# Kernel optimization log

Hardware: AMD Instinct MI355X
Metric: run time of the kernel (lower is better)

## Reference

```python
import jax, jax.numpy as jnp
import numpy as np

B, S, W, T = 16, 32, 32, 64
H2 = 512   # num_hidden*2: decoder state / encoder state size
Hf = 256   # vocab_nn hidden (= num_hidden)
F = 128    # vectorizer.vector_size
A = 128    # attn_hidden (= num_hidden // 2)
V = 32000  # vocab size; distribution over V+1 (last slot = OOV / -1 index)


def setup_inputs() -> dict:
    key = jax.random.key(0)
    ks = jax.random.split(key, 24)
    p = lambda k, shp, s=0.05: (jax.random.normal(k, shp) * s).astype(jnp.float32)
    d = {}
    d["text_states"] = p(ks[0], (B, S, W, H2), 0.5)
    d["sentence_states"] = p(ks[1], (B, S, H2), 0.5)
    d["text_length"] = jnp.clip(jax.random.randint(ks[2], (B, S), 0, W), 1, W)
    d["state"] = p(ks[3], (B, 2, H2), 0.5)
    d["summary"] = jax.random.randint(ks[4], (B, T), 0, V)
    d["summary_length"] = jnp.clip(jax.random.randint(ks[5], (B,), 0, T), 2, T)
    d["emb"] = p(ks[6], (V + 1, F), 0.02)            # vectorizer embedding
    d["W_cc"] = p(ks[7], (F + H2, F)); d["b_cc"] = jnp.zeros((F,), jnp.float32)
    d["Wx"] = p(ks[8], (F, 4 * H2)); d["Wh"] = p(ks[9], (H2, 4 * H2))
    d["b_lstm"] = jnp.zeros((4 * H2,), jnp.float32)
    d["W_a"] = p(ks[10], (2 * H2 + 1, A)); d["b_a"] = jnp.zeros((A,), jnp.float32)
    d["v_a"] = p(ks[11], (A,))
    d["W_rc"] = p(ks[12], (2 * H2, H2)); d["b_rc"] = jnp.zeros((H2,), jnp.float32)
    d["W1"] = p(ks[13], (2 * H2, Hf)); d["b1"] = jnp.zeros((Hf,), jnp.float32)
    d["W2"] = p(ks[14], (Hf, V + 1)); d["b2"] = jnp.zeros((V + 1,), jnp.float32)
    return d


def reference(text_states, sentence_states, text_length, state, summary,
              summary_length, emb, W_cc, b_cc, Wx, Wh, b_lstm,
              W_a, b_a, v_a, W_rc, b_rc, W1, b1, W2, b2):
    SW = S * W
    ws = text_states.reshape(B, SW, H2)  # word states, flattened source positions
    ss = jnp.broadcast_to(sentence_states[:, :, None, :], (B, S, W, H2)).reshape(B, SW, H2)
    cat_states = jnp.concatenate([ws, ss], -1)               # (B,SW,4H)
    mask = (jnp.arange(W) < text_length[:, :, None]).reshape(B, SW)
    Wa_word, Wa_out, wa_cov = W_a[:H2], W_a[H2:2 * H2], W_a[2 * H2]
    ws_a = ws @ Wa_word + b_a                                # step-invariant, (B,SW,A)

    def step(carry, xs):
        st, coverage, ctx, loss = carry
        tok_t, tok_tp1, t = xs
        valid = ((summary_length - t - 1) > 0).astype(jnp.float32)
        # CombineContext + LSTM decoder cell
        x = jnp.concatenate([emb[tok_t], ctx], 1) @ W_cc + b_cc
        h, c = st[:, 0], st[:, 1]
        gi, gf, gg, go = jnp.split(x @ Wx + h @ Wh + b_lstm, 4, axis=1)
        c_new = jax.nn.sigmoid(gf) * c + jax.nn.sigmoid(gi) * jnp.tanh(gg)
        out = jax.nn.sigmoid(go) * jnp.tanh(c_new)           # (B,2H)
        # hierarchical attention with coverage feature (input dim 4H+1)
        scores = jnp.tanh(ws_a + (out @ Wa_out)[:, None, :]
                          + coverage[:, :, None] * wa_cov) @ v_a
        attn = jax.nn.softmax(jnp.where(mask, scores, -1e9), axis=1)
        ctx4 = jnp.einsum('bn,bnd->bd', attn, cat_states)    # (B,4H)
        ctx_new = ctx4 @ W_rc + b_rc                         # ReduceContextVector -> (B,2H)
        # vocabulary distribution
        hid = jax.nn.relu(jnp.concatenate([ctx_new, out], 1) @ W1 + b1)
        vocab = jax.nn.softmax(hid @ W2 + b2, axis=1)        # (B,V+1)
        tgt = jnp.where(tok_tp1 == -1, V, tok_tp1)           # map_input_indices_
        logp = jnp.log(jnp.take_along_axis(vocab, tgt[:, None], 1)[:, 0])
        covloss = jnp.minimum(coverage, attn).sum(1)
        loss = loss + valid * (-logp + covloss)              # gamma = 1
        # scatter-back semantics of timestep_wrapper: invalid rows zeroed
        attn_m = attn * valid[:, None]
        st_new = jnp.stack([out, c_new], 1) * valid[:, None, None]
        return (st_new, coverage + attn_m, ctx_new * valid[:, None], loss), None

    coverage0 = jnp.zeros((B, SW), jnp.float32)
    ctx0 = jnp.zeros((B, H2), jnp.float32)
    loss0 = jnp.zeros((B,), jnp.float32)
    xs = (summary[:, :-1].T, summary[:, 1:].T, jnp.arange(T - 1))
    (_, _, _, loss), _ = jax.lax.scan(step, (state, coverage0, ctx0, loss0), xs)
    return loss / (summary_length.astype(jnp.float32) - 1.0)
```

## Files before the change

kernel.cpp:

```cpp
#include <hip/hip_runtime.h>
#include <math.h>

#define B 16
#define S 32
#define T 64
#define H2 512
#define Hf 256
#define F 128
#define A 128
#define V 32000
#define SW 1024
#define NSTEP 63
#define VP1 32001
#define NBLK 256

__device__ __forceinline__ float frcp(float x){ return __builtin_amdgcn_rcpf(x); }
__device__ __forceinline__ float fsigm(float x){ return frcp(1.f + __expf(-x)); }
__device__ __forceinline__ float ftanh_(float x){
    float e = __expf(-2.f*fabsf(x));
    float t = (1.f - e)*frcp(1.f + e);
    return x >= 0.f ? t : -t;
}
__device__ __forceinline__ void ast(float* p, float v){
    __hip_atomic_store(p, v, __ATOMIC_RELAXED, __HIP_MEMORY_SCOPE_AGENT);
}
__device__ __forceinline__ unsigned bfr(float x){
    unsigned u = __float_as_uint(x);
    return (u + 0x7fffu + ((u >> 16) & 1u)) >> 16;
}
__device__ __forceinline__ float blo(unsigned u){ return __uint_as_float(u << 16); }
__device__ __forceinline__ float bhi(unsigned u){ return __uint_as_float(u & 0xffff0000u); }

__device__ __forceinline__ void gbar(unsigned* arr, unsigned* rel, unsigned gen){
    asm volatile("s_waitcnt vmcnt(0) lgkmcnt(0)" ::: "memory");
    __syncthreads();
    if (blockIdx.x == 0){
        if (threadIdx.x > 0 && threadIdx.x < NBLK){
            while (__hip_atomic_load(&arr[threadIdx.x*32], __ATOMIC_RELAXED,
                                     __HIP_MEMORY_SCOPE_AGENT) < gen)
                __builtin_amdgcn_s_sleep(2);
        }
        __syncthreads();
        if (threadIdx.x == 0)
            __hip_atomic_store(rel, gen, __ATOMIC_RELAXED, __HIP_MEMORY_SCOPE_AGENT);
        __syncthreads();
    } else {
        if (threadIdx.x == 0){
            __hip_atomic_store(&arr[blockIdx.x*32], gen, __ATOMIC_RELAXED,
                               __HIP_MEMORY_SCOPE_AGENT);
            while (__hip_atomic_load(rel, __ATOMIC_RELAXED,
                                     __HIP_MEMORY_SCOPE_AGENT) < gen)
                __builtin_amdgcn_s_sleep(4);
        }
        __syncthreads();
    }
}

__global__ __launch_bounds__(256) void k_init0(
    const float* __restrict__ emb, const float* __restrict__ W_cc,
    const float* __restrict__ b_cc, const int* __restrict__ summary,
    float* __restrict__ xR, unsigned* __restrict__ cnt)
{
    int blk = blockIdx.x, tid = threadIdx.x;
    if (blk < 16){
        int b = blk;
        int tok = summary[b*T + 0];
        if (tid < F){
            float a = 0.f;
            for (int k = 0; k < F; ++k) a += emb[(size_t)tok*F + k]*W_cc[(size_t)k*F + tid];
            xR[b*F + tid] = a + b_cc[tid];
        }
    } else {
        for (int i = tid; i < 8256; i += 256) cnt[i] = 0u;
    }
}

__global__ __launch_bounds__(256) void k_wsa(
    const float* __restrict__ ws, const float* __restrict__ W_a, const float* __restrict__ b_a,
    float* __restrict__ ws_aT)
{
    __shared__ float wss2[512][20];
    int b = blockIdx.x, nt = blockIdx.y, tid = threadIdx.x;
    int n0 = nt*16;
    const float* wsrc = ws + ((size_t)(b*SW + n0))*H2;
    for (int i = tid; i < 16*512; i += 256){
        int n_l = i >> 9, k = i & 511;
        wss2[k][n_l] = wsrc[i];
    }
    __syncthreads();
    int a = tid & 127, nh = tid >> 7;
    float acc[8];
    float ba = b_a[a];
    #pragma unroll
    for (int j = 0; j < 8; ++j) acc[j] = ba;
    for (int k = 0; k < H2; ++k){
        float wa = W_a[k*A + a];
        const float4 u0 = *(const float4*)&wss2[k][nh*8];
        const float4 u1 = *(const float4*)&wss2[k][nh*8 + 4];
        acc[0] += u0.x*wa; acc[1] += u0.y*wa; acc[2] += u0.z*wa; acc[3] += u0.w*wa;
        acc[4] += u1.x*wa; acc[5] += u1.y*wa; acc[6] += u1.z*wa; acc[7] += u1.w*wa;
    }
    float* dst = ws_aT + ((size_t)(b*A + a))*SW + n0 + nh*8;
    #pragma unroll
    for (int j = 0; j < 8; ++j) dst[j] = acc[j];
}

__global__ __launch_bounds__(256) void k_wf(
    const float* __restrict__ W_rc, const float* __restrict__ b_rc,
    const float* __restrict__ W1, const float* __restrict__ b1,
    const float* __restrict__ W_cc,
    float* __restrict__ Wf, float* __restrict__ bf, float* __restrict__ bconst)
{
    __shared__ float wrc[4][512];
    int j = blockIdx.x, tid = threadIdx.x;
    if (j < 256){
        for (int i = tid; i < 2048; i += 256){
            int kk = i >> 9, r = i & 511;
            wrc[kk][r] = W_rc[((size_t)(j*4 + kk))*H2 + r];
        }
        __syncthreads();
        float a0=0,a1=0,a2=0,a3=0;
        for (int r = 0; r < 512; ++r){
            float w1 = W1[(size_t)r*Hf + tid];
            a0 += wrc[0][r]*w1; a1 += wrc[1][r]*w1; a2 += wrc[2][r]*w1; a3 += wrc[3][r]*w1;
        }
        Wf[((size_t)(j*4+0))*Hf + tid] = a0;
        Wf[((size_t)(j*4+1))*Hf + tid] = a1;
        Wf[((size_t)(j*4+2))*Hf + tid] = a2;
        Wf[((size_t)(j*4+3))*Hf + tid] = a3;
    } else {
        float acc = b1[tid];
        for (int r = 0; r < 512; ++r) acc += b_rc[r]*W1[(size_t)r*Hf + tid];
        bf[tid] = acc;
        if (tid < 128){
            float a = 0.f;
            for (int c = 0; c < H2; ++c) a += b_rc[c]*W_cc[(size_t)(F+c)*F + tid];
            bconst[tid] = a;
        }
    }
}

__global__ __launch_bounds__(128) void k_wrcc(
    const float* __restrict__ W_rc, const float* __restrict__ W_cc, float* __restrict__ WRCC)
{
    __shared__ float wr[512];
    int d = blockIdx.x, f = threadIdx.x;
    for (int i = f; i < 512; i += 128) wr[i] = W_rc[(size_t)d*H2 + i];
    __syncthreads();
    float a = 0.f;
    for (int c = 0; c < H2; ++c) a += wr[c]*W_cc[(size_t)(F+c)*F + f];
    WRCC[(size_t)d*F + f] = a;
}

__global__ __launch_bounds__(128) void k_embx(
    const int* __restrict__ summary, const float* __restrict__ emb,
    const float* __restrict__ W_cc, const float* __restrict__ b_cc,
    float* __restrict__ embx)
{
    __shared__ float er[128];
    int t = blockIdx.x, b = blockIdx.y, f = threadIdx.x;
    int tok = summary[b*T + t];
    er[f] = emb[(size_t)tok*F + f];
    __syncthreads();
    float a = b_cc[f];
    for (int k = 0; k < F; ++k) a += er[k]*W_cc[(size_t)k*F + f];
    embx[((size_t)t*B + b)*F + f] = a;
}

__global__ __launch_bounds__(1024) void k_packw2(
    const float* __restrict__ W2, unsigned* __restrict__ W2h)
{
    size_t idx = (size_t)blockIdx.x*1024 + threadIdx.x;
    int rp = (int)(idx >> 15), v = (int)(idx & 32767);
    float lo = (v < VP1) ? W2[(size_t)(2*rp)*VP1 + v] : 0.f;
    float hi = (v < VP1) ? W2[(size_t)(2*rp+1)*VP1 + v] : 0.f;
    W2h[idx] = bfr(lo) | (bfr(hi) << 16);
}
__global__ __launch_bounds__(1024) void k_packws(
    const float* __restrict__ ws, unsigned* __restrict__ wsh)
{
    size_t idx = (size_t)blockIdx.x*1024 + threadIdx.x;
    int b = (int)(idx >> 18), r = (int)(idx & 262143);
    int np = r >> 9, d = r & 511;
    float lo = ws[((size_t)b*SW + 2*np)*H2 + d];
    float hi = ws[((size_t)b*SW + 2*np+1)*H2 + d];
    wsh[idx] = bfr(lo) | (bfr(hi) << 16);
}
__global__ __launch_bounds__(1024) void k_packwsa(
    const float* __restrict__ ws_aT, unsigned* __restrict__ ws_aTh)
{
    size_t idx = (size_t)blockIdx.x*1024 + threadIdx.x;
    int b = (int)(idx >> 16), r = (int)(idx & 65535);
    int ap = r >> 10, n = r & 1023;
    float lo = ws_aT[((size_t)b*A + 2*ap)*SW + n];
    float hi = ws_aT[((size_t)b*A + 2*ap+1)*SW + n];
    ws_aTh[idx] = bfr(lo) | (bfr(hi) << 16);
}
__global__ __launch_bounds__(1024) void k_packwg(
    const float* __restrict__ Wx, const float* __restrict__ Wh,
    unsigned* __restrict__ wgh)
{
    size_t idx = (size_t)blockIdx.x*1024 + threadIdx.x;
    int kp = (int)(idx >> 11), cg = (int)(idx & 2047);
    int k0 = 2*kp, k1 = 2*kp + 1;
    float lo = (k0 < F) ? Wx[(size_t)k0*2048 + cg] : Wh[(size_t)(k0-F)*2048 + cg];
    float hi = (k1 < F) ? Wx[(size_t)k1*2048 + cg] : Wh[(size_t)(k1-F)*2048 + cg];
    wgh[idx] = bfr(lo) | (bfr(hi) << 16);
}

__global__ __launch_bounds__(512, 2) void k_persist(
    const float* __restrict__ ss,
    const int* __restrict__ text_length, const int* __restrict__ summary,
    const int* __restrict__ sumlen, const float* __restrict__ state,
    const unsigned* __restrict__ wgh, const float* __restrict__ b_lstm,
    const float* __restrict__ W_a, const float* __restrict__ v_a,
    const float* __restrict__ W1, const float* __restrict__ b2,
    const unsigned* __restrict__ W2h, const unsigned* __restrict__ wsh,
    const unsigned* __restrict__ ws_aTh,
    const float* __restrict__ Wf, const float* __restrict__ bf,
    const float* __restrict__ WRCC, const float* __restrict__ bconst,
    const float* __restrict__ embx,
    float* xR, float* outR, float* hidR, float* scoresR, float* c4R,
    float* woR, float* mpartR, float* spartR, float* m2R, float* s2R,
    float* tgtlogR, float* covlpR, float* d_out, unsigned* cnt)
{
    __shared__ unsigned W2L[16384];
    __shared__ unsigned wsaL[4096];
    __shared__ float BIG[15104];
    __shared__ float woOL[512];
    __shared__ float redS[576];
    __shared__ float red2[528];
    __shared__ float wo_l[128];
    __shared__ float wac_l[128], vas_l[128], b2_l[128];
    __shared__ float score_l[64], cov_l[64];
    __shared__ float c_l[128];
    __shared__ float gsum[528];
    __shared__ float asum_l[32];
    __shared__ float mred[136], sred[136], msc2[16];
    __shared__ float loss_l[16];
    __shared__ float misc[4];
    __shared__ int tl_l[32], sumlen_l[16], tgt_l[16];

    const int blk = blockIdx.x, tid = threadIdx.x;
    const int b_role = blk >> 4, sl = blk & 15;
    unsigned* arr = cnt;
    unsigned* rel = cnt + 8192;

    const int vl = tid & 127, rq = tid >> 7;
    const int dl = tid & 31, nq = tid >> 5;
    const int n3 = tid & 63, aq = tid >> 6;
    const int cc = tid & 31, kg = tid >> 5;

    unsigned wsr[32];
    #pragma unroll
    for (int j = 0; j < 32; ++j)
        wsr[j] = wsh[((size_t)b_role*512 + nq*32 + j)*512 + sl*32 + dl];
    unsigned wgr[20];
    if (blk < 64){
        const int CGg = (cc >> 3)*512 + blk*8 + (cc & 7);
        #pragma unroll
        for (int j = 0; j < 20; ++j)
            wgr[j] = wgh[(size_t)(kg*20 + j)*2048 + CGg];
    }
    #pragma unroll
    for (int q = 0; q < 32; ++q){
        int i = q*512 + tid;
        W2L[i] = W2h[(size_t)(i >> 7)*32768 + blk*128 + (i & 127)];
    }
    #pragma unroll
    for (int q = 0; q < 8; ++q){
        int i = q*512 + tid;
        wsaL[i] = ws_aTh[((size_t)(b_role*64 + (i >> 6)))*1024 + sl*64 + (i & 63)];
    }

    if (tid < 128){
        wac_l[tid] = W_a[(size_t)(2*H2)*A + tid];
        vas_l[tid] = v_a[tid];
        int v2 = blk*128 + tid;
        b2_l[tid] = (v2 < VP1) ? b2[v2] : 0.f;
    }
    if (tid < 32) tl_l[tid] = text_length[b_role*S + tid];
    if (tid < 16){ sumlen_l[tid] = sumlen[tid]; loss_l[tid] = 0.f; }
    if (tid < 64) cov_l[tid] = 0.f;
    if (blk < 64 && tid < 128){
        int b = tid >> 3, c = tid & 7;
        c_l[tid] = state[(size_t)b*2*H2 + H2 + blk*8 + c];
    }
    __syncthreads();

    unsigned gen = 0;
    for (int t = 0; t <= NSTEP; ++t){
        if (t >= 1){
            if (tid < 16) mred[tid] = mpartR[(size_t)(t-1)*256 + b_role*16 + tid];
            if (tid >= 16 && tid < 32) mred[tid] = spartR[(size_t)(t-1)*256 + b_role*16 + (tid-16)];
            __syncthreads();
            if (tid == 0){
                float M = -1e30f;
                for (int i = 0; i < 16; ++i) M = fmaxf(M, mred[i]);
                float Sv = 0.f;
                for (int i = 0; i < 16; ++i) Sv += mred[16+i]*__expf(mred[i]-M);
                misc[0] = M; misc[1] = frcp(Sv);
            }
            __syncthreads();
            if (tid < 64){
                float at = __expf(score_l[tid]-misc[0])*misc[1];
                float clp = fminf(cov_l[tid], at);
                float vm1 = (sumlen_l[b_role] - t > 0) ? 1.f : 0.f;
                cov_l[tid] += at*vm1;
                sred[tid] = clp;
            }
            __syncthreads();
            if (tid == 0){
                float s = 0.f;
                for (int i = 0; i < 64; ++i) s += sred[i];
                ast(&covlpR[(size_t)(t-1)*256 + b_role*16 + sl], s);
            }
            __syncthreads();
        }
        if (t < NSTEP && blk < 64){
            float* xh = BIG;
            const float* xb0 = xR + (size_t)t*B*F;
            const float* hb0 = outR + (size_t)(t > 0 ? t-1 : 0)*B*H2;
            #pragma unroll
            for (int q = 0; q < 20; ++q){
                int i = q*512 + tid;
                int b = i/640, k = i - b*640;
                float v;
                if (k < F) v = xb0[b*F + k];
                else if (t == 0) v = state[(size_t)b*2*H2 + (k - F)];
                else v = hb0[b*H2 + (k - F)] * ((sumlen_l[b] - t > 0) ? 1.f : 0.f);
                xh[i] = v;
            }
            __syncthreads();
            for (int b = 0; b < 16; ++b){
                const float* xb = &BIG[b*640 + kg*40];
                float s0 = 0.f, s1 = 0.f;
                #pragma unroll
                for (int j = 0; j < 20; ++j){
                    unsigned wu = wgr[j];
                    s0 = fmaf(xb[2*j],   blo(wu), s0);
                    s1 = fmaf(xb[2*j+1], bhi(wu), s1);
                }
                float p = s0 + s1;
                p += __shfl_xor(p, 32);
                if ((kg & 1) == 0)
                    BIG[10240 + (b*8 + (kg >> 1))*32 + cc] = p;
            }
            __syncthreads();
            {
                int b = tid >> 5, c2 = tid & 31;
                float s = 0.f;
                #pragma unroll
                for (int q = 0; q < 8; ++q) s += BIG[10240 + (b*8 + q)*32 + c2];
                gsum[b*33 + c2] = s;
            }
            __syncthreads();
            if (tid < 128){
                int b = tid >> 3, c = tid & 7, col = blk*8 + c;
                float gi = gsum[b*33 + c]      + b_lstm[col];
                float gf = gsum[b*33 + 8 + c]  + b_lstm[H2 + col];
                float gg = gsum[b*33 + 16 + c] + b_lstm[2*H2 + col];
                float go = gsum[b*33 + 24 + c] + b_lstm[3*H2 + col];
                float cold = c_l[tid];
                float cn = fsigm(gf)*cold + fsigm(gi)*ftanh_(gg);
                float o = fsigm(go)*ftanh_(cn);
                float valid = (sumlen_l[b] - t - 1 > 0) ? 1.f : 0.f;
                c_l[tid] = cn*valid;
                ast(&outR[(size_t)t*B*H2 + b*H2 + col], o);
            }
        }
        gen++; gbar(arr, rel, gen);

        if (t >= 1){
            if (tid < 16){ int tok = summary[tid*T + t]; tgt_l[tid] = (tok == -1) ? V : tok; }
            #pragma unroll
            for (int q = 0; q < 8; ++q){
                int idx = q*512 + tid;
                int r = idx >> 4, b = idx & 15;
                BIG[b*264 + r] = hidR[(size_t)(t-1)*B*Hf + idx];
            }
            __syncthreads();
            unsigned wreg[32];
            #pragma unroll
            for (int i = 0; i < 32; ++i) wreg[i] = W2L[(rq*32 + i)*128 + vl];
            for (int b = 0; b < 16; ++b){
                const float2* hb2 = (const float2*)&BIG[b*264 + rq*64];
                float a0 = 0.f, a1 = 0.f;
                #pragma unroll
                for (int i = 0; i < 32; ++i){
                    unsigned u = wreg[i];
                    float2 h = hb2[i];
                    a0 = fmaf(h.x, blo(u), a0);
                    a1 = fmaf(h.y, bhi(u), a1);
                }
                BIG[4224 + rq*2176 + vl*17 + b] = a0 + a1;
            }
            __syncthreads();
            #pragma unroll
            for (int j = 0; j < 4; ++j){
                int idx = tid*4 + j;
                int vl2 = idx >> 4, bb = idx & 15;
                float s = BIG[4224 + 0*2176 + vl2*17 + bb]
                        + BIG[4224 + 1*2176 + vl2*17 + bb]
                        + BIG[4224 + 2*2176 + vl2*17 + bb]
                        + BIG[4224 + 3*2176 + vl2*17 + bb];
                int v2 = blk*128 + vl2;
                float lg = (v2 < VP1) ? (s + b2_l[vl2]) : -1e30f;
                if (v2 < VP1 && v2 == tgt_l[bb])
                    ast(&tgtlogR[(size_t)(t-1)*16 + bb], lg);
                BIG[12928 + vl2*17 + bb] = lg;
            }
            __syncthreads();
            if (tid < 128){
                int b2i = tid & 15, grp = tid >> 4;
                float m = -1e30f;
                #pragma unroll
                for (int i = 0; i < 16; ++i) m = fmaxf(m, BIG[12928 + (grp*16+i)*17 + b2i]);
                mred[grp*17 + b2i] = m;
            }
            __syncthreads();
            if (tid < 16){
                float m = -1e30f;
                #pragma unroll
                for (int q = 0; q < 8; ++q) m = fmaxf(m, mred[q*17 + tid]);
                msc2[tid] = m;
            }
            __syncthreads();
            if (tid < 128){
                int b2i = tid & 15, grp = tid >> 4;
                float Mb = msc2[b2i];
                float s = 0.f;
                #pragma unroll
                for (int i = 0; i < 16; ++i) s += __expf(BIG[12928 + (grp*16+i)*17 + b2i] - Mb);
                sred[grp*17 + b2i] = s;
            }
            __syncthreads();
            if (tid < 16){
                float s = 0.f;
                #pragma unroll
                for (int q = 0; q < 8; ++q) s += sred[q*17 + tid];
                ast(&m2R[(size_t)(t-1)*B*256 + tid*256 + blk], msc2[tid]);
                ast(&s2R[(size_t)(t-1)*B*256 + tid*256 + blk], s);
            }
        }
        if (t < NSTEP && blk >= 128){
            int idx = blk - 128, bwo = idx >> 3, ah = idx & 7;
            woOL[tid] = outR[(size_t)t*B*H2 + bwo*H2 + tid];
            __syncthreads();
            {
                int a16 = tid & 15, kq2 = tid >> 4;
                float acc = 0.f;
                #pragma unroll
                for (int j = 0; j < 16; ++j){
                    int k = kq2*16 + j;
                    acc = fmaf(woOL[k], W_a[(size_t)(H2 + k)*A + ah*16 + a16], acc);
                }
                red2[a16*33 + kq2] = acc;
            }
            __syncthreads();
            if (tid < 16){
                float s = 0.f;
                #pragma unroll
                for (int q = 0; q < 32; ++q) s += red2[tid*33 + q];
                ast(&woR[(size_t)t*B*A + bwo*128 + ah*16 + tid], s);
            }
        }
        gen++; gbar(arr, rel, gen);

        if (t == NSTEP){
            if (blk == 255 && tid < 256){
                int tf = NSTEP - 1;
                int bb = tid >> 4, g = tid & 15;
                float mv[16];
                float m = -1e30f;
                #pragma unroll
                for (int j = 0; j < 16; ++j){
                    mv[j] = m2R[(size_t)tf*B*256 + bb*256 + g + j*16];
                    m = fmaxf(m, mv[j]);
                }
                #pragma unroll
                for (int off = 1; off < 16; off <<= 1) m = fmaxf(m, __shfl_xor(m, off, 16));
                float s = 0.f;
                #pragma unroll
                for (int j = 0; j < 16; ++j)
                    s += s2R[(size_t)tf*B*256 + bb*256 + g + j*16]*__expf(mv[j]-m);
                #pragma unroll
                for (int off = 1; off < 16; off <<= 1) s += __shfl_xor(s, off, 16);
                if (g == 0){
                    float cl = 0.f;
                    for (int q = 0; q < 16; ++q) cl += covlpR[(size_t)tf*256 + bb*16 + q];
                    float tlg = tgtlogR[(size_t)tf*16 + bb];
                    float logp = tlg - m - __logf(s);
                    float vld = (sumlen_l[bb] - tf - 1 > 0) ? 1.f : 0.f;
                    loss_l[bb] += vld*(-logp + cl);
                    d_out[bb] = loss_l[bb] / ((float)sumlen_l[bb] - 1.f);
                }
            }
            break;
        }

        {
            if (tid < 128) wo_l[tid] = woR[(size_t)t*B*A + b_role*128 + tid];
            __syncthreads();
            {
                float cv = cov_l[n3];
                float acc = 0.f;
                #pragma unroll
                for (int i = 0; i < 8; ++i){
                    unsigned u = wsaL[(aq*8 + i)*64 + n3];
                    int a0 = aq*16 + 2*i;
                    acc = fmaf(ftanh_(blo(u) + wo_l[a0] + cv*wac_l[a0]), vas_l[a0], acc);
                    acc = fmaf(ftanh_(bhi(u) + wo_l[a0+1] + cv*wac_l[a0+1]), vas_l[a0+1], acc);
                }
                redS[aq*72 + n3] = acc;
            }
            __syncthreads();
            if (tid < 64){
                float s = 0.f;
                #pragma unroll
                for (int q = 0; q < 8; ++q) s += redS[q*72 + tid];
                int nn = sl*64 + tid;
                float sc = ((nn & 31) < tl_l[nn >> 5]) ? s : -1e9f;
                score_l[tid] = sc;
                ast(&scoresR[(size_t)t*B*SW + b_role*SW + nn], sc);
            }
            __syncthreads();
            if (tid == 0){
                float m = score_l[0];
                for (int i = 1; i < 64; ++i) m = fmaxf(m, score_l[i]);
                float s = 0.f;
                for (int i = 0; i < 64; ++i) s += __expf(score_l[i]-m);
                ast(&mpartR[(size_t)t*256 + b_role*16 + sl], m);
                ast(&spartR[(size_t)t*256 + b_role*16 + sl], s);
            }
        }
        gen++; gbar(arr, rel, gen);

        {
            float* SC = BIG;
            float* AT = BIG + 1024;
            float* redc = BIG + 2048;
            #pragma unroll
            for (int q = 0; q < 2; ++q)
                SC[q*512 + tid] = scoresR[(size_t)t*B*SW + b_role*SW + q*512 + tid];
            if (tid < 16) mred[tid] = mpartR[(size_t)t*256 + b_role*16 + tid];
            if (tid >= 16 && tid < 32) mred[tid] = spartR[(size_t)t*256 + b_role*16 + (tid-16)];
            __syncthreads();
            if (tid == 0){
                float M = -1e30f;
                for (int i = 0; i < 16; ++i) M = fmaxf(M, mred[i]);
                float Sv = 0.f;
                for (int i = 0; i < 16; ++i) Sv += mred[16+i]*__expf(mred[i]-M);
                misc[0] = M; misc[1] = frcp(Sv);
            }
            __syncthreads();
            #pragma unroll
            for (int q = 0; q < 2; ++q){
                int n = q*512 + tid;
                AT[n] = __expf(SC[n]-misc[0])*misc[1];
            }
            __syncthreads();
            if (tid < 32){
                float s = 0.f;
                #pragma unroll
                for (int j = 0; j < 32; ++j) s += AT[tid*32 + ((j + tid) & 31)];
                asum_l[tid] = s;
            }
            {
                float acc0 = 0.f, acc1 = 0.f;
                const float2* at2 = (const float2*)&AT[nq*64];
                #pragma unroll
                for (int j = 0; j < 32; ++j){
                    unsigned u = wsr[j];
                    float2 av = at2[j];
                    acc0 = fmaf(av.x, blo(u), acc0);
                    acc1 = fmaf(av.y, bhi(u), acc1);
                }
                redc[nq*32 + dl] = acc0 + acc1;
            }
            __syncthreads();
            if (tid < 32){
                float s = 0.f;
                #pragma unroll
                for (int q = 0; q < 16; ++q) s += redc[q*32 + tid];
                ast(&c4R[(size_t)t*B*SW + b_role*SW + sl*32 + tid], s);
            } else if (tid < 64){
                int d2 = tid - 32;
                float s = 0.f;
                const float* ssb = ss + ((size_t)(b_role*S))*H2 + sl*32 + d2;
                #pragma unroll 4
                for (int s2 = 0; s2 < 32; ++s2)
                    s = fmaf(asum_l[s2], ssb[(size_t)s2*H2], s);
                ast(&c4R[(size_t)t*B*SW + b_role*SW + 512 + sl*32 + d2], s);
            }
        }
        gen++; gbar(arr, rel, gen);

        if (sl < 12){
            float* c4l = BIG;
            float* OL  = BIG + 1024;
            float* redd = BIG + 1536;
            #pragma unroll
            for (int q = 0; q < 2; ++q)
                c4l[q*512 + tid] = c4R[(size_t)t*B*SW + b_role*SW + q*512 + tid];
            if (tid < 512) OL[tid] = outR[(size_t)t*B*H2 + b_role*H2 + tid];
            __syncthreads();
            int cl = tid & 31, kq = tid >> 5;
            if (sl < 8){
                int col = sl*32 + cl;
                float acc = 0.f;
                const float* wp = Wf + (size_t)(kq*64)*Hf + col;
                #pragma unroll 4
                for (int i = 0; i < 64; ++i)
                    acc = fmaf(c4l[kq*64+i], wp[(size_t)i*Hf], acc);
                const float* w1p = W1 + (size_t)(H2 + kq*32)*Hf + col;
                #pragma unroll 4
                for (int i = 0; i < 32; ++i)
                    acc = fmaf(OL[kq*32+i], w1p[(size_t)i*Hf], acc);
                redd[kq*32 + cl] = acc;
                __syncthreads();
                if (tid < 32){
                    float z = 0.f;
                    #pragma unroll
                    for (int q = 0; q < 16; ++q) z += redd[q*32 + tid];
                    z += bf[sl*32 + tid];
                    ast(&hidR[(size_t)t*B*Hf + (sl*32 + tid)*16 + b_role], fmaxf(z, 0.f));
                }
            } else {
                int f = (sl-8)*32 + cl;
                float acc = 0.f;
                const float* wp = WRCC + (size_t)(kq*64)*F + f;
                #pragma unroll 4
                for (int i = 0; i < 64; ++i)
                    acc = fmaf(c4l[kq*64+i], wp[(size_t)i*F], acc);
                redd[kq*32 + cl] = acc;
                __syncthreads();
                if (tid < 32){
                    int f2 = (sl-8)*32 + tid;
                    float z = 0.f;
                    #pragma unroll
                    for (int q = 0; q < 16; ++q) z += redd[q*32 + tid];
                    float vld = (sumlen_l[b_role] - t - 1 > 0) ? 1.f : 0.f;
                    float xv = embx[((size_t)(t+1)*B + b_role)*F + f2] + vld*(z + bconst[f2]);
                    ast(&xR[(size_t)(t+1)*B*F + b_role*F + f2], xv);
                }
            }
        }
        if (t >= 1 && blk == 255 && tid < 256){
            int tf = t - 1;
            int bb = tid >> 4, g = tid & 15;
            float mv[16];
            float m = -1e30f;
            #pragma unroll
            for (int j = 0; j < 16; ++j){
                mv[j] = m2R[(size_t)tf*B*256 + bb*256 + g + j*16];
                m = fmaxf(m, mv[j]);
            }
            #pragma unroll
            for (int off = 1; off < 16; off <<= 1) m = fmaxf(m, __shfl_xor(m, off, 16));
            float s = 0.f;
            #pragma unroll
            for (int j = 0; j < 16; ++j)
                s += s2R[(size_t)tf*B*256 + bb*256 + g + j*16]*__expf(mv[j]-m);
            #pragma unroll
            for (int off = 1; off < 16; off <<= 1) s += __shfl_xor(s, off, 16);
            if (g == 0){
                float cl = 0.f;
                for (int q = 0; q < 16; ++q) cl += covlpR[(size_t)tf*256 + bb*16 + q];
                float tlg = tgtlogR[(size_t)tf*16 + bb];
                float logp = tlg - m - __logf(s);
                float vld = (sumlen_l[bb] - tf - 1 > 0) ? 1.f : 0.f;
                loss_l[bb] += vld*(-logp + cl);
            }
        }
        gen++; gbar(arr, rel, gen);
    }
}

extern "C" void kernel_launch(void* const* d_in, const int* in_sizes, int n_in,
                              void* d_out, int out_size, void* d_ws, size_t ws_size,
                              hipStream_t stream) {
    const float* text_states = (const float*)d_in[0];
    const float* sent_states = (const float*)d_in[1];
    const int*   text_length = (const int*)d_in[2];
    const float* state       = (const float*)d_in[3];
    const int*   summary     = (const int*)d_in[4];
    const int*   sumlen      = (const int*)d_in[5];
    const float* emb    = (const float*)d_in[6];
    const float* W_cc   = (const float*)d_in[7];
    const float* b_cc   = (const float*)d_in[8];
    const float* Wx     = (const float*)d_in[9];
    const float* Wh     = (const float*)d_in[10];
    const float* b_lstm = (const float*)d_in[11];
    const float* W_a    = (const float*)d_in[12];
    const float* b_a    = (const float*)d_in[13];
    const float* v_a    = (const float*)d_in[14];
    const float* W_rc   = (const float*)d_in[15];
    const float* b_rc   = (const float*)d_in[16];
    const float* W1     = (const float*)d_in[17];
    const float* b1     = (const float*)d_in[18];
    const float* W2     = (const float*)d_in[19];
    const float* b2     = (const float*)d_in[20];
    float* out = (float*)d_out;

    float* p = (float*)d_ws;
    float* ws_aT   = p; p += (size_t)B*A*SW;
    float* Wf      = p; p += (size_t)1024*Hf;
    float* bfv     = p; p += Hf;
    float* WRCC    = p; p += (size_t)1024*F;
    float* bconst  = p; p += F;
    float* embx    = p; p += (size_t)T*B*F;
    float* xR      = p; p += (size_t)(NSTEP+1)*B*F;
    float* outR    = p; p += (size_t)(NSTEP+1)*B*H2;
    float* hidR    = p; p += (size_t)(NSTEP+1)*B*Hf;
    float* scoresR = p; p += (size_t)(NSTEP+1)*B*SW;
    float* c4R     = p; p += (size_t)(NSTEP+1)*B*SW;
    float* woR     = p; p += (size_t)(NSTEP+1)*B*A;
    float* mpartR  = p; p += (size_t)(NSTEP+1)*256;
    float* spartR  = p; p += (size_t)(NSTEP+1)*256;
    float* m2R     = p; p += (size_t)(NSTEP+1)*B*256;
    float* s2R     = p; p += (size_t)(NSTEP+1)*B*256;
    float* tgtlogR = p; p += (size_t)(NSTEP+1)*16;
    float* covlpR  = p; p += (size_t)(NSTEP+1)*256;
    unsigned* cnt  = (unsigned*)p; p += 8256;
    unsigned* W2h    = (unsigned*)p; p += (size_t)128*32768;
    unsigned* wsh    = (unsigned*)p; p += (size_t)16*512*512;
    unsigned* ws_aTh = (unsigned*)p; p += (size_t)16*64*1024;
    unsigned* wgh    = (unsigned*)p; p += (size_t)320*2048;

    k_init0<<<17, 256, 0, stream>>>(emb, W_cc, b_cc, summary, xR, cnt);
    k_wsa<<<dim3(B, 64), 256, 0, stream>>>(text_states, W_a, b_a, ws_aT);
    k_wf<<<257, 256, 0, stream>>>(W_rc, b_rc, W1, b1, W_cc, Wf, bfv, bconst);
    k_wrcc<<<1024, 128, 0, stream>>>(W_rc, W_cc, WRCC);
    k_embx<<<dim3(T, B), 128, 0, stream>>>(summary, emb, W_cc, b_cc, embx);
    k_packw2<<<4096, 1024, 0, stream>>>(W2, W2h);
    k_packws<<<4096, 1024, 0, stream>>>(text_states, wsh);
    k_packwsa<<<1024, 1024, 0, stream>>>(ws_aT, ws_aTh);
    k_packwg<<<640, 1024, 0, stream>>>(Wx, Wh, wgh);
    k_persist<<<NBLK, 512, 0, stream>>>(
        sent_states, text_length, summary, sumlen, state,
        wgh, b_lstm, W_a, v_a, W1, b2,
        W2h, wsh, ws_aTh, Wf, bfv, WRCC, bconst, embx,
        xR, outR, hidR, scoresR, c4R, woR, mpartR, spartR, m2R, s2R,
        tgtlogR, covlpR, out, cnt);
}
```

Before: 4.692 ms.

## Fuse out@W_a into LSTM stage and merge vocab phase to drop grid barriers

The LSTM blocks now compute their partial out·W_a products right after producing their slice of the hidden state and write bf16-packed partials. The attention blocks reduce those partials directly, so the separate wo phase and its grid barrier go away. The vocab-logit/softmax-partial work moves into the same phase as the attention context, which removes one more barrier per step. The barrier release flag is spread over 8 cache lines and the spin sleeps are shortened. In exchange, wo is rounded through bf16 and the scratch buffer grows.

Result: faster. 4.489 ms (-4.3%).

```diff
diff --git a/kernel.cpp b/kernel.cpp
--- a/kernel.cpp
+++ b/kernel.cpp
@@ -24,6 +24,9 @@
 __device__ __forceinline__ void ast(float* p, float v){
     __hip_atomic_store(p, v, __ATOMIC_RELAXED, __HIP_MEMORY_SCOPE_AGENT);
 }
+__device__ __forceinline__ void astu(unsigned* p, unsigned v){
+    __hip_atomic_store(p, v, __ATOMIC_RELAXED, __HIP_MEMORY_SCOPE_AGENT);
+}
 __device__ __forceinline__ unsigned bfr(float x){
     unsigned u = __float_as_uint(x);
     return (u + 0x7fffu + ((u >> 16) & 1u)) >> 16;
@@ -38,19 +41,20 @@
         if (threadIdx.x > 0 && threadIdx.x < NBLK){
             while (__hip_atomic_load(&arr[threadIdx.x*32], __ATOMIC_RELAXED,
                                      __HIP_MEMORY_SCOPE_AGENT) < gen)
-                __builtin_amdgcn_s_sleep(2);
+                __builtin_amdgcn_s_sleep(1);
         }
         __syncthreads();
-        if (threadIdx.x == 0)
-            __hip_atomic_store(rel, gen, __ATOMIC_RELAXED, __HIP_MEMORY_SCOPE_AGENT);
+        if (threadIdx.x < 8)
+            __hip_atomic_store(&rel[threadIdx.x*32], gen, __ATOMIC_RELAXED,
+                               __HIP_MEMORY_SCOPE_AGENT);
         __syncthreads();
     } else {
         if (threadIdx.x == 0){
             __hip_atomic_store(&arr[blockIdx.x*32], gen, __ATOMIC_RELAXED,
                                __HIP_MEMORY_SCOPE_AGENT);
-            while (__hip_atomic_load(rel, __ATOMIC_RELAXED,
+            while (__hip_atomic_load(&rel[(blockIdx.x & 7)*32], __ATOMIC_RELAXED,
                                      __HIP_MEMORY_SCOPE_AGENT) < gen)
-                __builtin_amdgcn_s_sleep(4);
+                __builtin_amdgcn_s_sleep(1);
         }
         __syncthreads();
     }
@@ -71,7 +75,7 @@
             xR[b*F + tid] = a + b_cc[tid];
         }
     } else {
-        for (int i = tid; i < 8256; i += 256) cnt[i] = 0u;
+        for (int i = tid; i < 8704; i += 256) cnt[i] = 0u;
     }
 }
 
@@ -221,13 +225,12 @@
     const float* __restrict__ WRCC, const float* __restrict__ bconst,
     const float* __restrict__ embx,
     float* xR, float* outR, float* hidR, float* scoresR, float* c4R,
-    float* woR, float* mpartR, float* spartR, float* m2R, float* s2R,
+    unsigned* wopartH, float* mpartR, float* spartR, float* m2R, float* s2R,
     float* tgtlogR, float* covlpR, float* d_out, unsigned* cnt)
 {
     __shared__ unsigned W2L[16384];
     __shared__ unsigned wsaL[4096];
-    __shared__ float BIG[15104];
-    __shared__ float woOL[512];
+    __shared__ float BIG[15552];
     __shared__ float redS[576];
     __shared__ float red2[528];
     __shared__ float wo_l[128];
@@ -319,6 +322,13 @@
         }
         if (t < NSTEP && blk < 64){
             float* xh = BIG;
+            float* outloc = BIG + 14336;
+            float* waL = BIG + 14464;
+            {
+                int i2 = tid*2;
+                waL[i2]   = W_a[(size_t)(H2 + blk*8 + (i2 >> 7))*A + (i2 & 127)];
+                waL[i2+1] = W_a[(size_t)(H2 + blk*8 + ((i2+1) >> 7))*A + ((i2+1) & 127)];
+            }
             const float* xb0 = xR + (size_t)t*B*F;
             const float* hb0 = outR + (size_t)(t > 0 ? t-1 : 0)*B*H2;
             #pragma unroll
@@ -366,141 +376,51 @@
                 float o = fsigm(go)*ftanh_(cn);
                 float valid = (sumlen_l[b] - t - 1 > 0) ? 1.f : 0.f;
                 c_l[tid] = cn*valid;
+                outloc[tid] = o;
                 ast(&outR[(size_t)t*B*H2 + b*H2 + col], o);
             }
+            __syncthreads();
+            {
+                int o2 = tid*2;
+                int b = o2 >> 6, ap0 = o2 & 63;
+                #pragma unroll
+                for (int w = 0; w < 2; ++w){
+                    int ap = ap0 + w, a0 = ap*2;
+                    float acc0 = 0.f, acc1 = 0.f;
+                    #pragma unroll
+                    for (int j = 0; j < 8; ++j){
+                        float ov = outloc[b*8 + j];
+                        acc0 = fmaf(ov, waL[j*128 + a0],     acc0);
+                        acc1 = fmaf(ov, waL[j*128 + a0 + 1], acc1);
+                    }
+                    astu(&wopartH[(size_t)t*65536 + blk*1024 + b*64 + ap],
+                         bfr(acc0) | (bfr(acc1) << 16));
+                }
+            }
         }
         gen++; gbar(arr, rel, gen);
 
-        if (t >= 1){
-            if (tid < 16){ int tok = summary[tid*T + t]; tgt_l[tid] = (tok == -1) ? V : tok; }
-            #pragma unroll
-            for (int q = 0; q < 8; ++q){
-                int idx = q*512 + tid;
-                int r = idx >> 4, b = idx & 15;
-                BIG[b*264 + r] = hidR[(size_t)(t-1)*B*Hf + idx];
-            }
-            __syncthreads();
-            unsigned wreg[32];
-            #pragma unroll
-            for (int i = 0; i < 32; ++i) wreg[i] = W2L[(rq*32 + i)*128 + vl];
-            for (int b = 0; b < 16; ++b){
-                const float2* hb2 = (const float2*)&BIG[b*264 + rq*64];
-                float a0 = 0.f, a1 = 0.f;
-                #pragma unroll
-                for (int i = 0; i < 32; ++i){
-                    unsigned u = wreg[i];
-                    float2 h = hb2[i];
-                    a0 = fmaf(h.x, blo(u), a0);
-                    a1 = fmaf(h.y, bhi(u), a1);
-                }
-                BIG[4224 + rq*2176 + vl*17 + b] = a0 + a1;
-            }
-            __syncthreads();
-            #pragma unroll
-            for (int j = 0; j < 4; ++j){
-                int idx = tid*4 + j;
-                int vl2 = idx >> 4, bb = idx & 15;
-                float s = BIG[4224 + 0*2176 + vl2*17 + bb]
-                        + BIG[4224 + 1*2176 + vl2*17 + bb]
-                        + BIG[4224 + 2*2176 + vl2*17 + bb]
-                        + BIG[4224 + 3*2176 + vl2*17 + bb];
-                int v2 = blk*128 + vl2;
-                float lg = (v2 < VP1) ? (s + b2_l[vl2]) : -1e30f;
-                if (v2 < VP1 && v2 == tgt_l[bb])
-                    ast(&tgtlogR[(size_t)(t-1)*16 + bb], lg);
-                BIG[12928 + vl2*17 + bb] = lg;
-            }
-            __syncthreads();
-            if (tid < 128){
-                int b2i = tid & 15, grp = tid >> 4;
-                float m = -1e30f;
-                #pragma unroll
-                for (int i = 0; i < 16; ++i) m = fmaxf(m, BIG[12928 + (grp*16+i)*17 + b2i]);
-                mred[grp*17 + b2i] = m;
-            }
-            __syncthreads();
-            if (tid < 16){
-                float m = -1e30f;
-                #pragma unroll
-                for (int q = 0; q < 8; ++q) m = fmaxf(m, mred[q*17 + tid]);
-                msc2[tid] = m;
-            }
-            __syncthreads();
-            if (tid < 128){
-                int b2i = tid & 15, grp = tid >> 4;
-                float Mb = msc2[b2i];
-                float s = 0.f;
-                #pragma unroll
-                for (int i = 0; i < 16; ++i) s += __expf(BIG[12928 + (grp*16+i)*17 + b2i] - Mb);
-                sred[grp*17 + b2i] = s;
-            }
-            __syncthreads();
-            if (tid < 16){
-                float s = 0.f;
-                #pragma unroll
-                for (int q = 0; q < 8; ++q) s += sred[q*17 + tid];
-                ast(&m2R[(size_t)(t-1)*B*256 + tid*256 + blk], msc2[tid]);
-                ast(&s2R[(size_t)(t-1)*B*256 + tid*256 + blk], s);
-            }
-        }
-        if (t < NSTEP && blk >= 128){
-            int idx = blk - 128, bwo = idx >> 3, ah = idx & 7;
-            woOL[tid] = outR[(size_t)t*B*H2 + bwo*H2 + tid];
-            __syncthreads();
+        if (t < NSTEP){
             {
-                int a16 = tid & 15, kq2 = tid >> 4;
-                float acc = 0.f;
-                #pragma unroll
-                for (int j = 0; j < 16; ++j){
-                    int k = kq2*16 + j;
-                    acc = fmaf(woOL[k], W_a[(size_t)(H2 + k)*A + ah*16 + a16], acc);
-                }
-                red2[a16*33 + kq2] = acc;
-            }
-            __syncthreads();
-            if (tid < 16){
-                float s = 0.f;
-                #pragma unroll
-                for (int q = 0; q < 32; ++q) s += red2[tid*33 + q];
-                ast(&woR[(size_t)t*B*A + bwo*128 + ah*16 + tid], s);
-            }
-        }
-        gen++; gbar(arr, rel, gen);
-
-        if (t == NSTEP){
-            if (blk == 255 && tid < 256){
-                int tf = NSTEP - 1;
-                int bb = tid >> 4, g = tid & 15;
-                float mv[16];
-                float m = -1e30f;
-                #pragma unroll
-                for (int j = 0; j < 16; ++j){
-                    mv[j] = m2R[(size_t)tf*B*256 + bb*256 + g + j*16];
-                    m = fmaxf(m, mv[j]);
-                }
-                #pragma unroll
-                for (int off = 1; off < 16; off <<= 1) m = fmaxf(m, __shfl_xor(m, off, 16));
-                float s = 0.f;
-                #pragma unroll
-                for (int j = 0; j < 16; ++j)
-                    s += s2R[(size_t)tf*B*256 + bb*256 + g + j*16]*__expf(mv[j]-m);
-                #pragma unroll
-                for (int off = 1; off < 16; off <<= 1) s += __shfl_xor(s, off, 16);
-                if (g == 0){
-                    float cl = 0.f;
-                    for (int q = 0; q < 16; ++q) cl += covlpR[(size_t)tf*256 + bb*16 + q];
-                    float tlg = tgtlogR[(size_t)tf*16 + bb];
-                    float logp = tlg - m - __logf(s);
-                    float vld = (sumlen_l[bb] - tf - 1 > 0) ? 1.f : 0.f;
-                    loss_l[bb] += vld*(-logp + cl);
-                    d_out[bb] = loss_l[bb] / ((float)sumlen_l[bb] - 1.f);
-                }
-            }
-            break;
-        }
-
-        {
-            if (tid < 128) wo_l[tid] = woR[(size_t)t*B*A + b_role*128 + tid];
+                int ap = tid & 63, grp = tid >> 6;
+                const unsigned* wp = wopartH + (size_t)t*65536 + (size_t)(grp*8)*1024
+                                     + b_role*64 + ap;
+                float lo = 0.f, hi = 0.f;
+                #pragma unroll
+                for (int q = 0; q < 8; ++q){
+                    unsigned u = wp[(size_t)q*1024];
+                    lo += blo(u); hi += bhi(u);
+                }
+                red2[ap*8 + grp] = lo;
+                redS[ap*8 + grp] = hi;
+            }
+            __syncthreads();
+            if (tid < 64){
+                float lo = 0.f, hi = 0.f;
+                #pragma unroll
+                for (int q = 0; q < 8; ++q){ lo += red2[tid*8+q]; hi += redS[tid*8+q]; }
+                wo_l[tid*2] = lo; wo_l[tid*2+1] = hi;
+            }
             __syncthreads();
             {
                 float cv = cov_l[n3];
@@ -540,33 +460,51 @@
             float* SC = BIG;
             float* AT = BIG + 1024;
             float* redc = BIG + 2048;
-            #pragma unroll
-            for (int q = 0; q < 2; ++q)
-                SC[q*512 + tid] = scoresR[(size_t)t*B*SW + b_role*SW + q*512 + tid];
-            if (tid < 16) mred[tid] = mpartR[(size_t)t*256 + b_role*16 + tid];
-            if (tid >= 16 && tid < 32) mred[tid] = spartR[(size_t)t*256 + b_role*16 + (tid-16)];
-            __syncthreads();
-            if (tid == 0){
-                float M = -1e30f;
-                for (int i = 0; i < 16; ++i) M = fmaxf(M, mred[i]);
-                float Sv = 0.f;
-                for (int i = 0; i < 16; ++i) Sv += mred[16+i]*__expf(mred[i]-M);
-                misc[0] = M; misc[1] = frcp(Sv);
-            }
-            __syncthreads();
-            #pragma unroll
-            for (int q = 0; q < 2; ++q){
-                int n = q*512 + tid;
-                AT[n] = __expf(SC[n]-misc[0])*misc[1];
-            }
-            __syncthreads();
-            if (tid < 32){
-                float s = 0.f;
-                #pragma unroll
-                for (int j = 0; j < 32; ++j) s += AT[tid*32 + ((j + tid) & 31)];
-                asum_l[tid] = s;
-            }
-            {
+            float* hidL = BIG + 2560;
+            float* parts = BIG + 6784;
+            float* logitl = BIG;
+            if (t < NSTEP){
+                #pragma unroll
+                for (int q = 0; q < 2; ++q)
+                    SC[q*512 + tid] = scoresR[(size_t)t*B*SW + b_role*SW + q*512 + tid];
+                if (tid < 16) mred[tid] = mpartR[(size_t)t*256 + b_role*16 + tid];
+                if (tid >= 16 && tid < 32) mred[tid] = spartR[(size_t)t*256 + b_role*16 + (tid-16)];
+            }
+            if (t >= 1){
+                if (tid < 16){ int tok = summary[tid*T + t]; tgt_l[tid] = (tok == -1) ? V : tok; }
+                #pragma unroll
+                for (int q = 0; q < 8; ++q){
+                    int idx = q*512 + tid;
+                    int r = idx >> 4, b = idx & 15;
+                    hidL[b*264 + r] = hidR[(size_t)(t-1)*B*Hf + idx];
+                }
+            }
+            __syncthreads();
+            if (t < NSTEP){
+                if (tid == 0){
+                    float M = -1e30f;
+                    for (int i = 0; i < 16; ++i) M = fmaxf(M, mred[i]);
+                    float Sv = 0.f;
+                    for (int i = 0; i < 16; ++i) Sv += mred[16+i]*__expf(mred[i]-M);
+                    misc[0] = M; misc[1] = frcp(Sv);
+                }
+            }
+            __syncthreads();
+            if (t < NSTEP){
+                #pragma unroll
+                for (int q = 0; q < 2; ++q){
+                    int n = q*512 + tid;
+                    AT[n] = __expf(SC[n]-misc[0])*misc[1];
+                }
+            }
+            __syncthreads();
+            if (t < NSTEP){
+                if (tid < 32){
+                    float s = 0.f;
+                    #pragma unroll
+                    for (int j = 0; j < 32; ++j) s += AT[tid*32 + ((j + tid) & 31)];
+                    asum_l[tid] = s;
+                }
                 float acc0 = 0.f, acc1 = 0.f;
                 const float2* at2 = (const float2*)&AT[nq*64];
                 #pragma unroll
@@ -578,25 +516,93 @@
                 }
                 redc[nq*32 + dl] = acc0 + acc1;
             }
-            __syncthreads();
-            if (tid < 32){
-                float s = 0.f;
-                #pragma unroll
-                for (int q = 0; q < 16; ++q) s += redc[q*32 + tid];
-                ast(&c4R[(size_t)t*B*SW + b_role*SW + sl*32 + tid], s);
-            } else if (tid < 64){
-                int d2 = tid - 32;
-                float s = 0.f;
-                const float* ssb = ss + ((size_t)(b_role*S))*H2 + sl*32 + d2;
-                #pragma unroll 4
-                for (int s2 = 0; s2 < 32; ++s2)
-                    s = fmaf(asum_l[s2], ssb[(size_t)s2*H2], s);
-                ast(&c4R[(size_t)t*B*SW + b_role*SW + 512 + sl*32 + d2], s);
+            if (t >= 1){
+                unsigned wreg[32];
+                #pragma unroll
+                for (int i = 0; i < 32; ++i) wreg[i] = W2L[(rq*32 + i)*128 + vl];
+                for (int b = 0; b < 16; ++b){
+                    const float2* hb2 = (const float2*)&hidL[b*264 + rq*64];
+                    float a0 = 0.f, a1 = 0.f;
+                    #pragma unroll
+                    for (int i = 0; i < 32; ++i){
+                        unsigned u = wreg[i];
+                        float2 h = hb2[i];
+                        a0 = fmaf(h.x, blo(u), a0);
+                        a1 = fmaf(h.y, bhi(u), a1);
+                    }
+                    parts[rq*2176 + vl*17 + b] = a0 + a1;
+                }
+            }
+            __syncthreads();
+            if (t < NSTEP){
+                if (tid < 32){
+                    float s = 0.f;
+                    #pragma unroll
+                    for (int q = 0; q < 16; ++q) s += redc[q*32 + tid];
+                    ast(&c4R[(size_t)t*B*SW + b_role*SW + sl*32 + tid], s);
+                } else if (tid < 64){
+                    int d2 = tid - 32;
+                    float s = 0.f;
+                    const float* ssb = ss + ((size_t)(b_role*S))*H2 + sl*32 + d2;
+                    #pragma unroll 4
+                    for (int s2 = 0; s2 < 32; ++s2)
+                        s = fmaf(asum_l[s2], ssb[(size_t)s2*H2], s);
+                    ast(&c4R[(size_t)t*B*SW + b_role*SW + 512 + sl*32 + d2], s);
+                }
+            }
+            __syncthreads();
+            if (t >= 1){
+                #pragma unroll
+                for (int j = 0; j < 4; ++j){
+                    int idx = tid*4 + j;
+                    int vl2 = idx >> 4, bb = idx & 15;
+                    float s = parts[0*2176 + vl2*17 + bb]
+                            + parts[1*2176 + vl2*17 + bb]
+                            + parts[2*2176 + vl2*17 + bb]
+                            + parts[3*2176 + vl2*17 + bb];
+                    int v2 = blk*128 + vl2;
+                    float lg = (v2 < VP1) ? (s + b2_l[vl2]) : -1e30f;
+                    if (v2 < VP1 && v2 == tgt_l[bb])
+                        ast(&tgtlogR[(size_t)(t-1)*16 + bb], lg);
+                    logitl[vl2*17 + bb] = lg;
+                }
+                __syncthreads();
+                if (tid < 128){
+                    int b2i = tid & 15, grp = tid >> 4;
+                    float m = -1e30f;
+                    #pragma unroll
+                    for (int i = 0; i < 16; ++i) m = fmaxf(m, logitl[(grp*16+i)*17 + b2i]);
+                    mred[grp*17 + b2i] = m;
+                }
+                __syncthreads();
+                if (tid < 16){
+                    float m = -1e30f;
+                    #pragma unroll
+                    for (int q = 0; q < 8; ++q) m = fmaxf(m, mred[q*17 + tid]);
+                    msc2[tid] = m;
+                }
+                __syncthreads();
+                if (tid < 128){
+                    int b2i = tid & 15, grp = tid >> 4;
+                    float Mb = msc2[b2i];
+                    float s = 0.f;
+                    #pragma unroll
+                    for (int i = 0; i < 16; ++i) s += __expf(logitl[(grp*16+i)*17 + b2i] - Mb);
+                    sred[grp*17 + b2i] = s;
+                }
+                __syncthreads();
+                if (tid < 16){
+                    float s = 0.f;
+                    #pragma unroll
+                    for (int q = 0; q < 8; ++q) s += sred[q*17 + tid];
+                    ast(&m2R[(size_t)(t-1)*B*256 + tid*256 + blk], msc2[tid]);
+                    ast(&s2R[(size_t)(t-1)*B*256 + tid*256 + blk], s);
+                }
             }
         }
         gen++; gbar(arr, rel, gen);
 
-        if (sl < 12){
+        if (t < NSTEP && sl < 12){
             float* c4l = BIG;
             float* OL  = BIG + 1024;
             float* redd = BIG + 1536;
@@ -671,8 +677,10 @@
                 float logp = tlg - m - __logf(s);
                 float vld = (sumlen_l[bb] - tf - 1 > 0) ? 1.f : 0.f;
                 loss_l[bb] += vld*(-logp + cl);
-            }
-        }
+                if (t == NSTEP) d_out[bb] = loss_l[bb] / ((float)sumlen_l[bb] - 1.f);
+            }
+        }
+        if (t == NSTEP) break;
         gen++; gbar(arr, rel, gen);
     }
 }
@@ -715,18 +723,18 @@
     float* hidR    = p; p += (size_t)(NSTEP+1)*B*Hf;
     float* scoresR = p; p += (size_t)(NSTEP+1)*B*SW;
     float* c4R     = p; p += (size_t)(NSTEP+1)*B*SW;
-    float* woR     = p; p += (size_t)(NSTEP+1)*B*A;
     float* mpartR  = p; p += (size_t)(NSTEP+1)*256;
     float* spartR  = p; p += (size_t)(NSTEP+1)*256;
     float* m2R     = p; p += (size_t)(NSTEP+1)*B*256;
     float* s2R     = p; p += (size_t)(NSTEP+1)*B*256;
     float* tgtlogR = p; p += (size_t)(NSTEP+1)*16;
     float* covlpR  = p; p += (size_t)(NSTEP+1)*256;
-    unsigned* cnt  = (unsigned*)p; p += 8256;
+    unsigned* cnt  = (unsigned*)p; p += 8704;
     unsigned* W2h    = (unsigned*)p; p += (size_t)128*32768;
     unsigned* wsh    = (unsigned*)p; p += (size_t)16*512*512;
     unsigned* ws_aTh = (unsigned*)p; p += (size_t)16*64*1024;
     unsigned* wgh    = (unsigned*)p; p += (size_t)320*2048;
+    unsigned* wopartH= (unsigned*)p; p += (size_t)NSTEP*65536;
 
     k_init0<<<17, 256, 0, stream>>>(emb, W_cc, b_cc, summary, xR, cnt);
     k_wsa<<<dim3(B, 64), 256, 0, stream>>>(text_states, W_a, b_a, ws_aT);
@@ -741,6 +749,6 @@
         sent_states, text_length, summary, sumlen, state,
         wgh, b_lstm, W_a, v_a, W1, b2,
         W2h, wsh, ws_aTh, Wf, bfv, WRCC, bconst, embx,
-        xR, outR, hidR, scoresR, c4R, woR, mpartR, spartR, m2R, s2R,
+        xR, outR, hidR, scoresR, c4R, wopartH, mpartR, spartR, m2R, s2R,
         tgtlogR, covlpR, out, cnt);
 }
```
